# Optimization experiments

Hardware: AMD Instinct MI355X
Metric: run time of the kernel (lower is better)

The kernel has to match this reference:

```python
import jax, jax.numpy as jnp
import numpy as np

N = 100000   # total nodes
E = 1600000  # total edges
G = 1000     # graphs in batch
NPG = N // G # nodes per graph
IN = 128
HID = 128
LBL = 100
EMB = 32


def setup_inputs() -> dict:
    key = jax.random.key(0)
    ks = jax.random.split(key, 12)
    x = jax.random.normal(ks[0], (N, IN), dtype=jnp.float32)
    edge_index = jax.random.randint(ks[1], (2, E), 0, N, dtype=jnp.int32)
    drnl = jax.random.randint(ks[2], (N,), 0, LBL, dtype=jnp.int32)
    batch = (jnp.arange(N, dtype=jnp.int32) // NPG)
    target_local = jax.random.randint(ks[3], (2 * G,), 0, NPG, dtype=jnp.int32)
    ptr = jnp.arange(G + 1, dtype=jnp.int32) * NPG
    s = 0.02
    emb = s * jax.random.normal(ks[4], (LBL, EMB), dtype=jnp.float32)
    W1 = s * jax.random.normal(ks[5], (IN + EMB, HID), dtype=jnp.float32)
    b1 = jnp.zeros((HID,), jnp.float32)
    W2 = s * jax.random.normal(ks[6], (HID, HID), dtype=jnp.float32)
    b2 = jnp.zeros((HID,), jnp.float32)
    Wm1 = s * jax.random.normal(ks[7], (HID * 5, HID), dtype=jnp.float32)
    bm1 = jnp.zeros((HID,), jnp.float32)
    Wm2 = s * jax.random.normal(ks[8], (HID, 2), dtype=jnp.float32)
    bm2 = jnp.zeros((2,), jnp.float32)
    return {"x": x, "emb": emb, "W1": W1, "b1": b1, "W2": W2, "b2": b2,
            "Wm1": Wm1, "bm1": bm1, "Wm2": Wm2, "bm2": bm2,
            "edge_index": edge_index, "drnl": drnl, "batch": batch,
            "target_local": target_local, "ptr": ptr}


def gcn_conv(h, W, b, src, dst, n):
    # PyG GCNConv: linear, add self-loops, symmetric deg norm, scatter-add, bias
    hw = h @ W
    deg = jax.ops.segment_sum(jnp.ones(src.shape[0], hw.dtype), dst,
                              num_segments=n) + 1.0  # +1 for self loop
    dinv = jax.lax.rsqrt(deg)
    norm = dinv[src] * dinv[dst]          # [E]
    msg = hw[src] * norm[:, None]          # [E, hid] gather + scale
    agg = jax.ops.segment_sum(msg, dst, num_segments=n)
    agg = agg + hw * (dinv * dinv)[:, None]  # self-loop message
    return agg + b


def reference(x, emb, W1, b1, W2, b2, Wm1, bm1, Wm2, bm2,
              edge_index, drnl, batch, target_local, ptr):
    src, dst = edge_index[0], edge_index[1]
    n = x.shape[0]
    z = jnp.concatenate([x, emb[drnl]], axis=1)          # [N, in+32]
    z = jax.nn.relu(gcn_conv(z, W1, b1, src, dst, n))    # [N, hid]
    z = jax.nn.relu(gcn_conv(z, W2, b2, src, dst, n))    # [N, hid]
    g = ptr.shape[0] - 1
    h_pool = jax.ops.segment_max(z, batch, num_segments=g)  # global_max_pool
    uv = target_local.reshape(g, 2) + ptr[:-1, None]     # global node ids
    h_u = z[uv[:, 0]]
    h_v = z[uv[:, 1]]
    feats = jnp.concatenate([h_u, h_v, jnp.abs(h_u - h_v), h_u * h_v, h_pool],
                            axis=1)                      # [G, 5*hid]
    hidm = jax.nn.relu(feats @ Wm1 + bm1)
    logits = hidm @ Wm2 + bm2                            # [G, 2]
    return logits
```

## Files before the change

### kernel.cpp

```cpp
#include <hip/hip_runtime.h>
#include <hip/hip_bf16.h>
#include <math.h>

static inline size_t align_up(size_t x, size_t a) { return (x + a - 1) / a * a; }

typedef short bf16x8 __attribute__((ext_vector_type(8)));
typedef float f32x4 __attribute__((ext_vector_type(4)));
typedef unsigned short u16x8 __attribute__((ext_vector_type(8)));
typedef int i32x4 __attribute__((ext_vector_type(4)));


#define NBUCK 512
#define BCAP 8192

__global__ __launch_bounds__(256) void bin_kernel(
    const int* __restrict__ src, const int* __restrict__ dst,
    int* __restrict__ bcnt, unsigned* __restrict__ staging, int E) {
  __shared__ int lcnt[NBUCK];
  __shared__ int gbase[NBUCK];
  __shared__ int lidx[NBUCK];
  const int tid = threadIdx.x;
  const int base = blockIdx.x * 4096;
  lcnt[tid] = 0; lcnt[tid + 256] = 0;
  lidx[tid] = 0; lidx[tid + 256] = 0;
  __syncthreads();
#pragma unroll
  for (int j = 0; j < 4; ++j) {
    const int idx = base + j * 1024 + tid * 4;
    if (idx + 3 < E) {
      const i32x4 d4 = __builtin_nontemporal_load((const i32x4*)(dst + idx));
#pragma unroll
      for (int c = 0; c < 4; ++c) atomicAdd(&lcnt[d4[c] >> 8], 1);
    } else {
      for (int c = 0; c < 4; ++c)
        if (idx + c < E) atomicAdd(&lcnt[dst[idx + c] >> 8], 1);
    }
  }
  __syncthreads();
  {
    const int c0 = lcnt[tid];
    if (c0 > 0) gbase[tid] = atomicAdd(&bcnt[tid], c0);
    const int c1 = lcnt[tid + 256];
    if (c1 > 0) gbase[tid + 256] = atomicAdd(&bcnt[tid + 256], c1);
  }
  __syncthreads();
#pragma unroll
  for (int j = 0; j < 4; ++j) {
    const int idx = base + j * 1024 + tid * 4;
    if (idx + 3 < E) {
      const i32x4 d4 = __builtin_nontemporal_load((const i32x4*)(dst + idx));
      const i32x4 s4 = __builtin_nontemporal_load((const i32x4*)(src + idx));
#pragma unroll
      for (int c = 0; c < 4; ++c) {
        const int d = d4[c];
        const int bkt = d >> 8;
        const int i = atomicAdd(&lidx[bkt], 1);
        const int pos = gbase[bkt] + i;
        if (pos < BCAP)
          staging[(size_t)bkt * BCAP + pos] =
              ((unsigned)s4[c] << 8) | ((unsigned)d & 255u);
      }
    } else {
      for (int c = 0; c < 4; ++c) {
        if (idx + c < E) {
          const int d = dst[idx + c];
          const int bkt = d >> 8;
          const int i = atomicAdd(&lidx[bkt], 1);
          const int pos = gbase[bkt] + i;
          if (pos < BCAP)
            staging[(size_t)bkt * BCAP + pos] =
                ((unsigned)src[idx + c] << 8) | ((unsigned)d & 255u);
        }
      }
    }
  }
}


__global__ __launch_bounds__(256) void csr_kernel(
    const unsigned* __restrict__ staging, const int* __restrict__ bcnt,
    int* __restrict__ rowptr, float* __restrict__ dinv, int* __restrict__ esrc,
    int N, int E) {
  __shared__ int sb[NBUCK];
  __shared__ int c1[256];
  __shared__ int off[256];
  __shared__ int sm[256];
  const int b = blockIdx.x;
  const int tid = threadIdx.x;
  sb[tid] = bcnt[tid];
  sb[tid + 256] = bcnt[tid + 256];
  __syncthreads();
  for (int o = 1; o < NBUCK; o <<= 1) {
    const int x0 = (tid >= o) ? sb[tid - o] : 0;
    const int x1 = (tid + 256 >= o) ? sb[tid + 256 - o] : 0;
    __syncthreads();
    sb[tid] += x0;
    sb[tid + 256] += x1;
    __syncthreads();
  }
  const int cnt = min(bcnt[b], BCAP);
  const int base = sb[b] - bcnt[b];
  if (b == 0 && tid == 0) rowptr[N] = E;
  const unsigned* sp = staging + (size_t)b * BCAP;
  c1[tid] = 0;
  __syncthreads();
  for (int i = tid; i < cnt; i += 256) {
    atomicAdd(&c1[sp[i] & 255u], 1);
  }
  __syncthreads();
  const int deg = c1[tid];
  sm[tid] = deg;
  __syncthreads();
  for (int o = 1; o < 256; o <<= 1) {
    const int x = (tid >= o) ? sm[tid - o] : 0;
    __syncthreads();
    sm[tid] += x;
    __syncthreads();
  }
  off[tid] = sm[tid] - deg;
  const int node = b * 256 + tid;
  if (node < N) {
    rowptr[node] = base + off[tid];
    dinv[node] = rsqrtf((float)(deg + 1));
  }
  c1[tid] = 0;
  __syncthreads();
  for (int i = tid; i < cnt; i += 256) {
    const unsigned pr = sp[i];
    const int d8 = (int)(pr & 255u);
    const int idx = atomicAdd(&c1[d8], 1);
    esrc[base + off[d8] + idx] = (int)(pr >> 8);
  }
}


__device__ __forceinline__ void bf16_split(float x, unsigned short& hi, unsigned short& lo) {
  unsigned u = __float_as_uint(x);
  unsigned r = (u + 0x7fffu + ((u >> 16) & 1u)) & 0xffff0000u;
  hi = (unsigned short)(r >> 16);
  float rem = x - __uint_as_float(r);
  unsigned u2 = __float_as_uint(rem);
  unsigned r2 = u2 + 0x7fffu + ((u2 >> 16) & 1u);
  lo = (unsigned short)(r2 >> 16);
}

__device__ __forceinline__ unsigned short bf16_rtn(float x) {
  unsigned u = __float_as_uint(x);
  return (unsigned short)((u + 0x7fffu + ((u >> 16) & 1u)) >> 16);
}

__device__ __forceinline__ float bf16_to_f(unsigned short v) {
  return __uint_as_float((unsigned)v << 16);
}

__global__ void wsplit_kernel(const float* __restrict__ W1, const float* __restrict__ W2,
                              unsigned short* __restrict__ w1hi, unsigned short* __restrict__ w1lo,
                              unsigned short* __restrict__ w2hi, unsigned short* __restrict__ w2lo) {
  int i = blockIdx.x * blockDim.x + threadIdx.x;
  const int t1 = 160 * 128;
  const int t2 = 128 * 128;
  const float* W;
  unsigned short *whi, *wlo;
  if (i < t1) {
    W = W1; whi = w1hi; wlo = w1lo;
  } else {
    i -= t1;
    if (i >= t2) return;
    W = W2; whi = w2hi; wlo = w2lo;
  }
  int k = i >> 7;
  int n = i & 127;
  unsigned short h, l;
  bf16_split(W[i], h, l);
  size_t idx = ((size_t)(((k >> 5) * 128 + n) * 4 + ((k >> 3) & 3)) << 3) + (k & 7);
  whi[idx] = h;
  wlo[idx] = l;
}


__global__ __launch_bounds__(512) void gemm_mfma_kernel(
    const float* __restrict__ A, const float* __restrict__ emb,
    const int* __restrict__ drnl,
    const unsigned short* __restrict__ whi, const unsigned short* __restrict__ wlo,
    unsigned short* __restrict__ outb, int n, int K) {
  __shared__ unsigned short smem[16896];
  const int tid = threadIdx.x;
  const int row0 = blockIdx.x * 128;
  const int w = tid >> 6;
  const int l = tid & 63;
  const int r = l & 15;
  const int q = l >> 4;
  const int grow = row0 + (w << 4) + r;
  const bool rowok = grow < n;
  const int nks = K >> 5;

  int embrow = 0;
  if (K > 128 && rowok) embrow = drnl[grow];

  f32x4 acc[8];
#pragma unroll
  for (int ct = 0; ct < 8; ++ct) {
    acc[ct][0] = 0.f; acc[ct][1] = 0.f; acc[ct][2] = 0.f; acc[ct][3] = 0.f;
  }

  u16x8 bst_h = *(const u16x8*)(whi + (size_t)tid * 8);
  u16x8 bst_l = *(const u16x8*)(wlo + (size_t)tid * 8);

  for (int ks = 0; ks < nks; ++ks) {
    const int k0 = (ks << 5) + (q << 3);
    float4 a0 = make_float4(0.f, 0.f, 0.f, 0.f), a1 = a0;
    if (rowok) {
      if (k0 < 128) {
        const float* ap = A + (size_t)grow * 128 + k0;
        a0 = *(const float4*)ap;
        a1 = *(const float4*)(ap + 4);
      } else {
        const float* ep = emb + (size_t)embrow * 32 + (k0 - 128);
        a0 = *(const float4*)ep;
        a1 = *(const float4*)(ep + 4);
      }
    }
    bf16x8 ah, al;
    {
      unsigned short h, lo_;
      bf16_split(a0.x, h, lo_); ah[0] = (short)h; al[0] = (short)lo_;
      bf16_split(a0.y, h, lo_); ah[1] = (short)h; al[1] = (short)lo_;
      bf16_split(a0.z, h, lo_); ah[2] = (short)h; al[2] = (short)lo_;
      bf16_split(a0.w, h, lo_); ah[3] = (short)h; al[3] = (short)lo_;
      bf16_split(a1.x, h, lo_); ah[4] = (short)h; al[4] = (short)lo_;
      bf16_split(a1.y, h, lo_); ah[5] = (short)h; al[5] = (short)lo_;
      bf16_split(a1.z, h, lo_); ah[6] = (short)h; al[6] = (short)lo_;
      bf16_split(a1.w, h, lo_); ah[7] = (short)h; al[7] = (short)lo_;
    }

    if (ks) __syncthreads();
    *(u16x8*)&smem[tid * 8] = bst_h;
    *(u16x8*)&smem[4096 + tid * 8] = bst_l;
    __syncthreads();

    if (ks + 1 < nks) {
      bst_h = *(const u16x8*)(whi + (size_t)(ks + 1) * 4096 + (size_t)tid * 8);
      bst_l = *(const u16x8*)(wlo + (size_t)(ks + 1) * 4096 + (size_t)tid * 8);
    }

#pragma unroll
    for (int ct = 0; ct < 8; ++ct) {
      const int boff = ((ct << 4) + r) * 32 + (q << 3);
      const bf16x8 bh = *(const bf16x8*)&smem[boff];
      const bf16x8 bl = *(const bf16x8*)&smem[4096 + boff];
      acc[ct] = __builtin_amdgcn_mfma_f32_16x16x32_bf16(ah, bh, acc[ct], 0, 0, 0);
      acc[ct] = __builtin_amdgcn_mfma_f32_16x16x32_bf16(al, bh, acc[ct], 0, 0, 0);
      acc[ct] = __builtin_amdgcn_mfma_f32_16x16x32_bf16(ah, bl, acc[ct], 0, 0, 0);
    }
  }

  __syncthreads();
#pragma unroll
  for (int ct = 0; ct < 8; ++ct) {
    const int col = (ct << 4) + r;
#pragma unroll
    for (int j = 0; j < 4; ++j) {
      const int row = (w << 4) + (q << 2) + j;
      smem[row * 132 + col] = bf16_rtn(acc[ct][j]);
    }
  }
  __syncthreads();
#pragma unroll
  for (int p = 0; p < 4; ++p) {
    const int idx = p * 512 + tid;
    const int row = idx >> 4;
    const int c8 = (idx & 15) * 8;
    const int gr = row0 + row;
    if (gr < n) {
      u16x8 v = *(const u16x8*)&smem[row * 132 + c8];
      *(u16x8*)(outb + (size_t)gr * 128 + c8) = v;
    }
  }
}


__global__ __launch_bounds__(512) void gemm_bf16a_kernel(
    const unsigned short* __restrict__ Ab,
    const unsigned short* __restrict__ whi, const unsigned short* __restrict__ wlo,
    unsigned short* __restrict__ outb, int n) {
  __shared__ unsigned short smem[16896];
  const int tid = threadIdx.x;
  const int row0 = blockIdx.x * 128;
  const int w = tid >> 6;
  const int l = tid & 63;
  const int r = l & 15;
  const int q = l >> 4;
  const int grow = row0 + (w << 4) + r;
  const bool rowok = grow < n;
  const int nks = 4;

  f32x4 acc[8];
#pragma unroll
  for (int ct = 0; ct < 8; ++ct) {
    acc[ct][0] = 0.f; acc[ct][1] = 0.f; acc[ct][2] = 0.f; acc[ct][3] = 0.f;
  }

  u16x8 bst_h = *(const u16x8*)(whi + (size_t)tid * 8);
  u16x8 bst_l = *(const u16x8*)(wlo + (size_t)tid * 8);

  for (int ks = 0; ks < nks; ++ks) {
    const int k0 = (ks << 5) + (q << 3);
    bf16x8 ah = {0,0,0,0,0,0,0,0};
    if (rowok) ah = *(const bf16x8*)(Ab + (size_t)grow * 128 + k0);

    if (ks) __syncthreads();
    *(u16x8*)&smem[tid * 8] = bst_h;
    *(u16x8*)&smem[4096 + tid * 8] = bst_l;
    __syncthreads();

    if (ks + 1 < nks) {
      bst_h = *(const u16x8*)(whi + (size_t)(ks + 1) * 4096 + (size_t)tid * 8);
      bst_l = *(const u16x8*)(wlo + (size_t)(ks + 1) * 4096 + (size_t)tid * 8);
    }

#pragma unroll
    for (int ct = 0; ct < 8; ++ct) {
      const int boff = ((ct << 4) + r) * 32 + (q << 3);
      const bf16x8 bh = *(const bf16x8*)&smem[boff];
      const bf16x8 bl = *(const bf16x8*)&smem[4096 + boff];
      acc[ct] = __builtin_amdgcn_mfma_f32_16x16x32_bf16(ah, bh, acc[ct], 0, 0, 0);
      acc[ct] = __builtin_amdgcn_mfma_f32_16x16x32_bf16(ah, bl, acc[ct], 0, 0, 0);
    }
  }

  __syncthreads();
#pragma unroll
  for (int ct = 0; ct < 8; ++ct) {
    const int col = (ct << 4) + r;
#pragma unroll
    for (int j = 0; j < 4; ++j) {
      const int row = (w << 4) + (q << 2) + j;
      smem[row * 132 + col] = bf16_rtn(acc[ct][j]);
    }
  }
  __syncthreads();
#pragma unroll
  for (int p = 0; p < 4; ++p) {
    const int idx = p * 512 + tid;
    const int row = idx >> 4;
    const int c8 = (idx & 15) * 8;
    const int gr = row0 + row;
    if (gr < n) {
      u16x8 v = *(const u16x8*)&smem[row * 132 + c8];
      *(u16x8*)(outb + (size_t)gr * 128 + c8) = v;
    }
  }
}


__global__ __launch_bounds__(256) void agg_kernel(
    const unsigned* __restrict__ hwb, const int* __restrict__ rowptr,
    const int* __restrict__ esrc, const float* __restrict__ dinv,
    const float* __restrict__ bias, unsigned* __restrict__ zb, int n) {
  const int widx = (blockIdx.x * blockDim.x + threadIdx.x) >> 6;
  if (widx >= n) return;
  const int wid = __builtin_amdgcn_readfirstlane(widx);
  const int lane = threadIdx.x & 63;
  const int start = rowptr[wid];
  const int end = rowptr[wid + 1];
  const float dn = dinv[wid];
  float ax = 0.f, ay = 0.f;
  int e = start;
  for (; e + 8 <= end; e += 8) {
    int s[8];
#pragma unroll
    for (int k = 0; k < 8; ++k) s[k] = esrc[e + k];
    unsigned u[8];
#pragma unroll
    for (int k = 0; k < 8; ++k) u[k] = hwb[(size_t)s[k] * 64 + lane];
    float dv[8];
#pragma unroll
    for (int k = 0; k < 8; ++k) dv[k] = dinv[s[k]];
#pragma unroll
    for (int k = 0; k < 8; ++k) {
      const float wk = dv[k] * dn;
      ax = fmaf(__uint_as_float(u[k] << 16), wk, ax);
      ay = fmaf(__uint_as_float(u[k] & 0xffff0000u), wk, ay);
    }
  }
  for (; e < end; ++e) {
    const int s0 = esrc[e];
    const float w0 = dinv[s0] * dn;
    const unsigned u0 = hwb[(size_t)s0 * 64 + lane];
    ax = fmaf(__uint_as_float(u0 << 16), w0, ax);
    ay = fmaf(__uint_as_float(u0 & 0xffff0000u), w0, ay);
  }
  const float sw = dn * dn;
  const unsigned us = hwb[(size_t)wid * 64 + lane];
  ax = fmaf(__uint_as_float(us << 16), sw, ax);
  ay = fmaf(__uint_as_float(us & 0xffff0000u), sw, ay);
  const float2 bb = ((const float2*)bias)[lane];
  float ox = ax + bb.x, oy = ay + bb.y;
  ox = ox > 0.f ? ox : 0.f;
  oy = oy > 0.f ? oy : 0.f;
  const unsigned pw = ((unsigned)bf16_rtn(oy) << 16) | (unsigned)bf16_rtn(ox);
  zb[(size_t)wid * 64 + lane] = pw;
}


__global__ __launch_bounds__(128) void final_kernel(
    const unsigned short* __restrict__ zb, const int* __restrict__ tloc,
    const int* __restrict__ ptr,
    const float* __restrict__ Wm1, const float* __restrict__ bm1,
    const float* __restrict__ Wm2, const float* __restrict__ bm2,
    float* __restrict__ out, int npg) {
  __shared__ float feats[640];
  __shared__ float hid[128];
  const int g = blockIdx.x;
  const int t = threadIdx.x;
  const unsigned short* zbk = zb + (size_t)g * npg * 128;
  float m = -INFINITY;
  for (int r = 0; r < npg; ++r) m = fmaxf(m, bf16_to_f(zbk[(size_t)r * 128 + t]));
  feats[512 + t] = m;
  const int base = ptr[g];
  const int u = base + tloc[2 * g];
  const int v = base + tloc[2 * g + 1];
  const float hu = bf16_to_f(zb[(size_t)u * 128 + t]);
  const float hv = bf16_to_f(zb[(size_t)v * 128 + t]);
  feats[t] = hu;
  feats[128 + t] = hv;
  feats[256 + t] = fabsf(hu - hv);
  feats[384 + t] = hu * hv;
  __syncthreads();
  float acc = bm1[t];
#pragma unroll 8
  for (int k = 0; k < 640; ++k) acc = fmaf(feats[k], Wm1[(size_t)k * 128 + t], acc);
  hid[t] = acc > 0.f ? acc : 0.f;
  __syncthreads();
  if (t < 2) {
    float a = bm2[t];
    for (int j = 0; j < 128; ++j) a = fmaf(hid[j], Wm2[j * 2 + t], a);
    out[g * 2 + t] = a;
  }
}


extern "C" void kernel_launch(void* const* d_in, const int* in_sizes, int n_in,
                              void* d_out, int out_size, void* d_ws, size_t ws_size,
                              hipStream_t stream) {
  const float* x   = (const float*)d_in[0];
  const float* emb = (const float*)d_in[1];
  const float* W1  = (const float*)d_in[2];
  const float* b1  = (const float*)d_in[3];
  const float* W2  = (const float*)d_in[4];
  const float* b2  = (const float*)d_in[5];
  const float* Wm1 = (const float*)d_in[6];
  const float* bm1 = (const float*)d_in[7];
  const float* Wm2 = (const float*)d_in[8];
  const float* bm2 = (const float*)d_in[9];
  const int* eidx  = (const int*)d_in[10];
  const int* drnl  = (const int*)d_in[11];
  const int* tloc  = (const int*)d_in[13];
  const int* ptr   = (const int*)d_in[14];
  float* out = (float*)d_out;

  const int N = in_sizes[11];
  const int E = in_sizes[10] / 2;
  const int G = in_sizes[13] / 2;
  const int NPG = N / G;
  const int* srcp = eidx;
  const int* dstp = eidx + E;

  char* w = (char*)d_ws;
  size_t o = 0;
  auto alloc = [&](size_t bytes) {
    void* p = w + o;
    o = align_up(o + bytes, 256);
    return p;
  };
  int*   rowptr = (int*)alloc((size_t)(N + 1) * 4);
  float* dinv   = (float*)alloc((size_t)N * 4);
  int*   bcnt   = (int*)alloc(NBUCK * 4);
  int*   esrc   = (int*)alloc((size_t)E * 4);
  unsigned short* hwb  = (unsigned short*)alloc((size_t)N * 128 * 2);
  unsigned short* zb1  = (unsigned short*)alloc((size_t)N * 128 * 2);
  unsigned short* zb2  = (unsigned short*)alloc((size_t)N * 128 * 2);
  unsigned* staging = (unsigned*)zb2;
  unsigned short* w1hi = (unsigned short*)alloc((size_t)160 * 128 * 2);
  unsigned short* w1lo = (unsigned short*)alloc((size_t)160 * 128 * 2);
  unsigned short* w2hi = (unsigned short*)alloc((size_t)128 * 128 * 2);
  unsigned short* w2lo = (unsigned short*)alloc((size_t)128 * 128 * 2);

  const int nch = (E + 4095) / 4096;
  const int nbk = (N + 255) / 256;

  hipMemsetAsync(bcnt, 0, NBUCK * 4, stream);
  bin_kernel<<<nch, 256, 0, stream>>>(srcp, dstp, bcnt, staging, E);
  csr_kernel<<<nbk, 256, 0, stream>>>(staging, bcnt, rowptr, dinv, esrc, N, E);

  wsplit_kernel<<<(160 * 128 + 128 * 128 + 255) / 256, 256, 0, stream>>>(
      W1, W2, w1hi, w1lo, w2hi, w2lo);

  gemm_mfma_kernel<<<(N + 127) / 128, 512, 0, stream>>>(x, emb, drnl, w1hi, w1lo, hwb, N, 160);
  agg_kernel<<<(N * 64 + 255) / 256, 256, 0, stream>>>((const unsigned*)hwb, rowptr, esrc,
                                                       dinv, b1, (unsigned*)zb1, N);
  gemm_bf16a_kernel<<<(N + 127) / 128, 512, 0, stream>>>(zb1, w2hi, w2lo, hwb, N);
  agg_kernel<<<(N * 64 + 255) / 256, 256, 0, stream>>>((const unsigned*)hwb, rowptr, esrc,
                                                       dinv, b2, (unsigned*)zb2, N);
  final_kernel<<<G, 128, 0, stream>>>(zb2, tloc, ptr, Wm1, bm1, Wm2, bm2, out, NPG);
}
```

Before: 270.2 us.

## Fuse weight split into bin kernel, double-buffer GEMM weights, single-pass binning

Merges the weight bf16-split work into extra blocks of the bin kernel, which removes one launch. The binning pass now reads src/dst from global memory once and buffers the records in shared memory, instead of reading dst twice. Both GEMM kernels double-buffer the weight tiles in LDS with a fully unrolled K loop, cutting one barrier per step. The final kernel's max-pool reads packed bf16 pairs and splits rows across two half-blocks. The price is more shared memory in the bin kernel (about 24KB), which may lower its occupancy.

Result: faster. 258.5 us (-4.3%).

```diff
diff --git a/kernel.cpp b/kernel.cpp
--- a/kernel.cpp
+++ b/kernel.cpp
@@ -9,44 +9,72 @@
 typedef unsigned short u16x8 __attribute__((ext_vector_type(8)));
 typedef int i32x4 __attribute__((ext_vector_type(4)));
 
-
 #define NBUCK 512
 #define BCAP 8192
 
+
+__device__ __forceinline__ void bf16_split(float x, unsigned short& hi, unsigned short& lo) {
+  unsigned u = __float_as_uint(x);
+  unsigned r = (u + 0x7fffu + ((u >> 16) & 1u)) & 0xffff0000u;
+  hi = (unsigned short)(r >> 16);
+  float rem = x - __uint_as_float(r);
+  unsigned u2 = __float_as_uint(rem);
+  unsigned r2 = u2 + 0x7fffu + ((u2 >> 16) & 1u);
+  lo = (unsigned short)(r2 >> 16);
+}
+
+__device__ __forceinline__ unsigned short bf16_rtn(float x) {
+  unsigned u = __float_as_uint(x);
+  return (unsigned short)((u + 0x7fffu + ((u >> 16) & 1u)) >> 16);
+}
+
+__device__ __forceinline__ float bf16_to_f(unsigned short v) {
+  return __uint_as_float((unsigned)v << 16);
+}
+
+
 __global__ __launch_bounds__(256) void bin_kernel(
     const int* __restrict__ src, const int* __restrict__ dst,
-    int* __restrict__ bcnt, unsigned* __restrict__ staging, int E) {
+    int* __restrict__ bcnt, unsigned* __restrict__ staging, int E, int nch,
+    const float* __restrict__ W1, const float* __restrict__ W2,
+    unsigned short* __restrict__ w1hi, unsigned short* __restrict__ w1lo,
+    unsigned short* __restrict__ w2hi, unsigned short* __restrict__ w2lo) {
+  const int tid = threadIdx.x;
+  if ((int)blockIdx.x >= nch) {
+    int i = ((int)blockIdx.x - nch) * 256 + tid;
+    const int t1 = 160 * 128;
+    const int t2 = 128 * 128;
+    const float* W;
+    unsigned short *whi, *wlo;
+    if (i < t1) {
+      W = W1; whi = w1hi; wlo = w1lo;
+    } else {
+      i -= t1;
+      if (i >= t2) return;
+      W = W2; whi = w2hi; wlo = w2lo;
+    }
+    int k = i >> 7;
+    int n = i & 127;
+    unsigned short h, l;
+    bf16_split(W[i], h, l);
+    size_t idx = ((size_t)(((k >> 5) * 128 + n) * 4 + ((k >> 3) & 3)) << 3) + (k & 7);
+    whi[idx] = h;
+    wlo[idx] = l;
+    return;
+  }
   __shared__ int lcnt[NBUCK];
   __shared__ int gbase[NBUCK];
   __shared__ int lidx[NBUCK];
-  const int tid = threadIdx.x;
+  __shared__ unsigned srec[4096];
+  __shared__ unsigned short sbkt[4096];
   const int base = blockIdx.x * 4096;
   lcnt[tid] = 0; lcnt[tid + 256] = 0;
   lidx[tid] = 0; lidx[tid + 256] = 0;
   __syncthreads();
 #pragma unroll
   for (int j = 0; j < 4; ++j) {
-    const int idx = base + j * 1024 + tid * 4;
-    if (idx + 3 < E) {
-      const i32x4 d4 = __builtin_nontemporal_load((const i32x4*)(dst + idx));
-#pragma unroll
-      for (int c = 0; c < 4; ++c) atomicAdd(&lcnt[d4[c] >> 8], 1);
-    } else {
-      for (int c = 0; c < 4; ++c)
-        if (idx + c < E) atomicAdd(&lcnt[dst[idx + c] >> 8], 1);
-    }
-  }
-  __syncthreads();
-  {
-    const int c0 = lcnt[tid];
-    if (c0 > 0) gbase[tid] = atomicAdd(&bcnt[tid], c0);
-    const int c1 = lcnt[tid + 256];
-    if (c1 > 0) gbase[tid + 256] = atomicAdd(&bcnt[tid + 256], c1);
-  }
-  __syncthreads();
-#pragma unroll
-  for (int j = 0; j < 4; ++j) {
-    const int idx = base + j * 1024 + tid * 4;
+    const int slot = j * 1024 + tid * 4;
+    const int idx = base + slot;
     if (idx + 3 < E) {
       const i32x4 d4 = __builtin_nontemporal_load((const i32x4*)(dst + idx));
       const i32x4 s4 = __builtin_nontemporal_load((const i32x4*)(src + idx));
@@ -54,23 +82,42 @@
       for (int c = 0; c < 4; ++c) {
         const int d = d4[c];
         const int bkt = d >> 8;
-        const int i = atomicAdd(&lidx[bkt], 1);
-        const int pos = gbase[bkt] + i;
-        if (pos < BCAP)
-          staging[(size_t)bkt * BCAP + pos] =
-              ((unsigned)s4[c] << 8) | ((unsigned)d & 255u);
+        atomicAdd(&lcnt[bkt], 1);
+        srec[slot + c] = ((unsigned)s4[c] << 8) | ((unsigned)d & 255u);
+        sbkt[slot + c] = (unsigned short)bkt;
       }
     } else {
       for (int c = 0; c < 4; ++c) {
         if (idx + c < E) {
           const int d = dst[idx + c];
           const int bkt = d >> 8;
-          const int i = atomicAdd(&lidx[bkt], 1);
-          const int pos = gbase[bkt] + i;
-          if (pos < BCAP)
-            staging[(size_t)bkt * BCAP + pos] =
-                ((unsigned)src[idx + c] << 8) | ((unsigned)d & 255u);
+          atomicAdd(&lcnt[bkt], 1);
+          srec[slot + c] = ((unsigned)src[idx + c] << 8) | ((unsigned)d & 255u);
+          sbkt[slot + c] = (unsigned short)bkt;
+        } else {
+          sbkt[slot + c] = 0xFFFFu;
         }
+      }
+    }
+  }
+  __syncthreads();
+  {
+    const int c0 = lcnt[tid];
+    if (c0 > 0) gbase[tid] = atomicAdd(&bcnt[tid], c0);
+    const int c1 = lcnt[tid + 256];
+    if (c1 > 0) gbase[tid + 256] = atomicAdd(&bcnt[tid + 256], c1);
+  }
+  __syncthreads();
+#pragma unroll
+  for (int j = 0; j < 4; ++j) {
+    const int slot = j * 1024 + tid * 4;
+#pragma unroll
+    for (int c = 0; c < 4; ++c) {
+      const int bkt = sbkt[slot + c];
+      if (bkt != 0xFFFF) {
+        const int i = atomicAdd(&lidx[bkt], 1);
+        const int pos = gbase[bkt] + i;
+        if (pos < BCAP) staging[(size_t)bkt * BCAP + pos] = srec[slot + c];
       }
     }
   }
@@ -134,55 +181,11 @@
 }
 
 
-__device__ __forceinline__ void bf16_split(float x, unsigned short& hi, unsigned short& lo) {
-  unsigned u = __float_as_uint(x);
-  unsigned r = (u + 0x7fffu + ((u >> 16) & 1u)) & 0xffff0000u;
-  hi = (unsigned short)(r >> 16);
-  float rem = x - __uint_as_float(r);
-  unsigned u2 = __float_as_uint(rem);
-  unsigned r2 = u2 + 0x7fffu + ((u2 >> 16) & 1u);
-  lo = (unsigned short)(r2 >> 16);
-}
-
-__device__ __forceinline__ unsigned short bf16_rtn(float x) {
-  unsigned u = __float_as_uint(x);
-  return (unsigned short)((u + 0x7fffu + ((u >> 16) & 1u)) >> 16);
-}
-
-__device__ __forceinline__ float bf16_to_f(unsigned short v) {
-  return __uint_as_float((unsigned)v << 16);
-}
-
-__global__ void wsplit_kernel(const float* __restrict__ W1, const float* __restrict__ W2,
-                              unsigned short* __restrict__ w1hi, unsigned short* __restrict__ w1lo,
-                              unsigned short* __restrict__ w2hi, unsigned short* __restrict__ w2lo) {
-  int i = blockIdx.x * blockDim.x + threadIdx.x;
-  const int t1 = 160 * 128;
-  const int t2 = 128 * 128;
-  const float* W;
-  unsigned short *whi, *wlo;
-  if (i < t1) {
-    W = W1; whi = w1hi; wlo = w1lo;
-  } else {
-    i -= t1;
-    if (i >= t2) return;
-    W = W2; whi = w2hi; wlo = w2lo;
-  }
-  int k = i >> 7;
-  int n = i & 127;
-  unsigned short h, l;
-  bf16_split(W[i], h, l);
-  size_t idx = ((size_t)(((k >> 5) * 128 + n) * 4 + ((k >> 3) & 3)) << 3) + (k & 7);
-  whi[idx] = h;
-  wlo[idx] = l;
-}
-
-
 __global__ __launch_bounds__(512) void gemm_mfma_kernel(
     const float* __restrict__ A, const float* __restrict__ emb,
     const int* __restrict__ drnl,
     const unsigned short* __restrict__ whi, const unsigned short* __restrict__ wlo,
-    unsigned short* __restrict__ outb, int n, int K) {
+    unsigned short* __restrict__ outb, int n) {
   __shared__ unsigned short smem[16896];
   const int tid = threadIdx.x;
   const int row0 = blockIdx.x * 128;
@@ -192,10 +195,10 @@
   const int q = l >> 4;
   const int grow = row0 + (w << 4) + r;
   const bool rowok = grow < n;
-  const int nks = K >> 5;
+  const int NKS = 5;
 
   int embrow = 0;
-  if (K > 128 && rowok) embrow = drnl[grow];
+  if (rowok) embrow = drnl[grow];
 
   f32x4 acc[8];
 #pragma unroll
@@ -205,8 +208,14 @@
 
   u16x8 bst_h = *(const u16x8*)(whi + (size_t)tid * 8);
   u16x8 bst_l = *(const u16x8*)(wlo + (size_t)tid * 8);
-
-  for (int ks = 0; ks < nks; ++ks) {
+  *(u16x8*)&smem[tid * 8] = bst_h;
+  *(u16x8*)&smem[4096 + tid * 8] = bst_l;
+  bst_h = *(const u16x8*)(whi + 4096 + (size_t)tid * 8);
+  bst_l = *(const u16x8*)(wlo + 4096 + (size_t)tid * 8);
+  __syncthreads();
+
+#pragma unroll
+  for (int ks = 0; ks < NKS; ++ks) {
     const int k0 = (ks << 5) + (q << 3);
     float4 a0 = make_float4(0.f, 0.f, 0.f, 0.f), a1 = a0;
     if (rowok) {
@@ -233,28 +242,29 @@
       bf16_split(a1.w, h, lo_); ah[7] = (short)h; al[7] = (short)lo_;
     }
 
-    if (ks) __syncthreads();
-    *(u16x8*)&smem[tid * 8] = bst_h;
-    *(u16x8*)&smem[4096 + tid * 8] = bst_l;
-    __syncthreads();
-
-    if (ks + 1 < nks) {
-      bst_h = *(const u16x8*)(whi + (size_t)(ks + 1) * 4096 + (size_t)tid * 8);
-      bst_l = *(const u16x8*)(wlo + (size_t)(ks + 1) * 4096 + (size_t)tid * 8);
-    }
-
+    if (ks + 1 < NKS) {
+      const int nxt = ((ks + 1) & 1) * 8192;
+      *(u16x8*)&smem[nxt + tid * 8] = bst_h;
+      *(u16x8*)&smem[nxt + 4096 + tid * 8] = bst_l;
+      if (ks + 2 < NKS) {
+        bst_h = *(const u16x8*)(whi + (size_t)(ks + 2) * 4096 + (size_t)tid * 8);
+        bst_l = *(const u16x8*)(wlo + (size_t)(ks + 2) * 4096 + (size_t)tid * 8);
+      }
+    }
+
+    const int cur = (ks & 1) * 8192;
 #pragma unroll
     for (int ct = 0; ct < 8; ++ct) {
-      const int boff = ((ct << 4) + r) * 32 + (q << 3);
+      const int boff = cur + ((ct << 4) + r) * 32 + (q << 3);
       const bf16x8 bh = *(const bf16x8*)&smem[boff];
-      const bf16x8 bl = *(const bf16x8*)&smem[4096 + boff];
+      const bf16x8 bl = *(const bf16x8*)&smem[boff + 4096];
       acc[ct] = __builtin_amdgcn_mfma_f32_16x16x32_bf16(ah, bh, acc[ct], 0, 0, 0);
       acc[ct] = __builtin_amdgcn_mfma_f32_16x16x32_bf16(al, bh, acc[ct], 0, 0, 0);
       acc[ct] = __builtin_amdgcn_mfma_f32_16x16x32_bf16(ah, bl, acc[ct], 0, 0, 0);
     }
-  }
-
-  __syncthreads();
+    __syncthreads();
+  }
+
 #pragma unroll
   for (int ct = 0; ct < 8; ++ct) {
     const int col = (ct << 4) + r;
@@ -292,7 +302,7 @@
   const int q = l >> 4;
   const int grow = row0 + (w << 4) + r;
   const bool rowok = grow < n;
-  const int nks = 4;
+  const int NKS = 4;
 
   f32x4 acc[8];
 #pragma unroll
@@ -302,33 +312,40 @@
 
   u16x8 bst_h = *(const u16x8*)(whi + (size_t)tid * 8);
   u16x8 bst_l = *(const u16x8*)(wlo + (size_t)tid * 8);
-
-  for (int ks = 0; ks < nks; ++ks) {
+  *(u16x8*)&smem[tid * 8] = bst_h;
+  *(u16x8*)&smem[4096 + tid * 8] = bst_l;
+  bst_h = *(const u16x8*)(whi + 4096 + (size_t)tid * 8);
+  bst_l = *(const u16x8*)(wlo + 4096 + (size_t)tid * 8);
+  __syncthreads();
+
+#pragma unroll
+  for (int ks = 0; ks < NKS; ++ks) {
     const int k0 = (ks << 5) + (q << 3);
     bf16x8 ah = {0,0,0,0,0,0,0,0};
     if (rowok) ah = *(const bf16x8*)(Ab + (size_t)grow * 128 + k0);
 
-    if (ks) __syncthreads();
-    *(u16x8*)&smem[tid * 8] = bst_h;
-    *(u16x8*)&smem[4096 + tid * 8] = bst_l;
-    __syncthreads();
-
-    if (ks + 1 < nks) {
-      bst_h = *(const u16x8*)(whi + (size_t)(ks + 1) * 4096 + (size_t)tid * 8);
-      bst_l = *(const u16x8*)(wlo + (size_t)(ks + 1) * 4096 + (size_t)tid * 8);
-    }
-
+    if (ks + 1 < NKS) {
+      const int nxt = ((ks + 1) & 1) * 8192;
+      *(u16x8*)&smem[nxt + tid * 8] = bst_h;
+      *(u16x8*)&smem[nxt + 4096 + tid * 8] = bst_l;
+      if (ks + 2 < NKS) {
+        bst_h = *(const u16x8*)(whi + (size_t)(ks + 2) * 4096 + (size_t)tid * 8);
+        bst_l = *(const u16x8*)(wlo + (size_t)(ks + 2) * 4096 + (size_t)tid * 8);
+      }
+    }
+
+    const int cur = (ks & 1) * 8192;
 #pragma unroll
     for (int ct = 0; ct < 8; ++ct) {
-      const int boff = ((ct << 4) + r) * 32 + (q << 3);
+      const int boff = cur + ((ct << 4) + r) * 32 + (q << 3);
       const bf16x8 bh = *(const bf16x8*)&smem[boff];
-      const bf16x8 bl = *(const bf16x8*)&smem[4096 + boff];
+      const bf16x8 bl = *(const bf16x8*)&smem[boff + 4096];
       acc[ct] = __builtin_amdgcn_mfma_f32_16x16x32_bf16(ah, bh, acc[ct], 0, 0, 0);
       acc[ct] = __builtin_amdgcn_mfma_f32_16x16x32_bf16(ah, bl, acc[ct], 0, 0, 0);
     }
-  }
-
-  __syncthreads();
+    __syncthreads();
+  }
+
 #pragma unroll
   for (int ct = 0; ct < 8; ++ct) {
     const int col = (ct << 4) + r;
@@ -411,12 +428,22 @@
     float* __restrict__ out, int npg) {
   __shared__ float feats[640];
   __shared__ float hid[128];
+  __shared__ float pm[2][128];
   const int g = blockIdx.x;
   const int t = threadIdx.x;
-  const unsigned short* zbk = zb + (size_t)g * npg * 128;
-  float m = -INFINITY;
-  for (int r = 0; r < npg; ++r) m = fmaxf(m, bf16_to_f(zbk[(size_t)r * 128 + t]));
-  feats[512 + t] = m;
+  {
+    const unsigned* zrow = (const unsigned*)(zb + (size_t)g * npg * 128);
+    const int p = t & 63;
+    const int h = t >> 6;
+    float m0 = -INFINITY, m1 = -INFINITY;
+    for (int r = h; r < npg; r += 2) {
+      const unsigned u = zrow[(size_t)r * 64 + p];
+      m0 = fmaxf(m0, __uint_as_float(u << 16));
+      m1 = fmaxf(m1, __uint_as_float(u & 0xffff0000u));
+    }
+    pm[h][2 * p] = m0;
+    pm[h][2 * p + 1] = m1;
+  }
   const int base = ptr[g];
   const int u = base + tloc[2 * g];
   const int v = base + tloc[2 * g + 1];
@@ -426,6 +453,8 @@
   feats[128 + t] = hv;
   feats[256 + t] = fabsf(hu - hv);
   feats[384 + t] = hu * hv;
+  __syncthreads();
+  feats[512 + t] = fmaxf(pm[0][t], pm[1][t]);
   __syncthreads();
   float acc = bm1[t];
 #pragma unroll 8
@@ -487,16 +516,15 @@
   unsigned short* w2lo = (unsigned short*)alloc((size_t)128 * 128 * 2);
 
   const int nch = (E + 4095) / 4096;
+  const int nwsp = (160 * 128 + 128 * 128 + 255) / 256;
   const int nbk = (N + 255) / 256;
 
   hipMemsetAsync(bcnt, 0, NBUCK * 4, stream);
-  bin_kernel<<<nch, 256, 0, stream>>>(srcp, dstp, bcnt, staging, E);
+  bin_kernel<<<nch + nwsp, 256, 0, stream>>>(srcp, dstp, bcnt, staging, E, nch,
+                                             W1, W2, w1hi, w1lo, w2hi, w2lo);
   csr_kernel<<<nbk, 256, 0, stream>>>(staging, bcnt, rowptr, dinv, esrc, N, E);
 
-  wsplit_kernel<<<(160 * 128 + 128 * 128 + 255) / 256, 256, 0, stream>>>(
-      W1, W2, w1hi, w1lo, w2hi, w2lo);
-
-  gemm_mfma_kernel<<<(N + 127) / 128, 512, 0, stream>>>(x, emb, drnl, w1hi, w1lo, hwb, N, 160);
+  gemm_mfma_kernel<<<(N + 127) / 128, 512, 0, stream>>>(x, emb, drnl, w1hi, w1lo, hwb, N);
   agg_kernel<<<(N * 64 + 255) / 256, 256, 0, stream>>>((const unsigned*)hwb, rowptr, esrc,
                                                        dinv, b1, (unsigned*)zb1, N);
   gemm_bf16a_kernel<<<(N + 127) / 128, 512, 0, stream>>>(zb1, w2hi, w2lo, hwb, N);
```
